# Performance work log

Hardware: AMD Instinct MI355X
Metric: run time of the kernel (lower is better)

The kernel has to match this reference:

```python
import jax, jax.numpy as jnp
import numpy as np

USER_NUM = 100000
ITEM_NUM = 100000
N = USER_NUM + ITEM_NUM
D = 64
N_EDGES = 3200000
N_LAYERS = 3
LAYER_CL = 1
EPS = 0.2


def setup_inputs() -> dict:
    key = jax.random.key(0)
    k1, k2, k3, k4, k5, k6 = jax.random.split(key, 6)
    user_emb = jax.random.normal(k1, (USER_NUM, D), dtype=jnp.float32)
    item_emb = jax.random.normal(k2, (ITEM_NUM, D), dtype=jnp.float32)
    adj_src = jax.random.randint(k3, (N_EDGES,), 0, N, dtype=jnp.int64)
    adj_dst = jax.random.randint(k4, (N_EDGES,), 0, N, dtype=jnp.int64)
    adj_vals = jax.random.uniform(k5, (N_EDGES,), dtype=jnp.float32)
    noise = jax.random.uniform(k6, (N_LAYERS, N, D), dtype=jnp.float32)
    return {"user_emb": user_emb, "item_emb": item_emb, "adj_src": adj_src,
            "adj_dst": adj_dst, "adj_vals": adj_vals, "noise": noise}


def reference(user_emb, item_emb, adj_src, adj_dst, adj_vals, noise):
    # ego_embeddings = cat([user_emb, item_emb])  -> [N, D]
    ego = jnp.concatenate([user_emb, item_emb], axis=0)
    acc = jnp.zeros_like(ego)
    cl = ego
    for k in range(N_LAYERS):
        # sparse.mm: out[dst] += val * ego[src]
        msg = ego[adj_src] * adj_vals[:, None]          # [E, D]
        ego = jax.ops.segment_sum(msg, adj_dst, num_segments=N)
        # perturbed noise injection: ego += sign(ego) * F.normalize(noise, dim=-1) * eps
        rn = noise[k]
        rn = rn / jnp.maximum(jnp.linalg.norm(rn, axis=-1, keepdims=True), 1e-12)
        ego = ego + jnp.sign(ego) * rn * EPS
        acc = acc + ego
        if k == LAYER_CL - 1:
            cl = ego
    final = acc / N_LAYERS  # mean over stacked layer outputs
    return (final[:USER_NUM], final[USER_NUM:], cl[:USER_NUM], cl[USER_NUM:])
```

## Files before the change

kernel.cpp:

```cpp
#include <hip/hip_runtime.h>

#define USER_NUM 100000
#define ITEM_NUM 100000
#define NN 200000
#define DIM 64
#define EPSV 0.2f

#define NB 196
#define BSH 10
#define NPB 1024
#define CH 4096
#define PER 16
#define SRC_MASK 0x3FFFF

__global__ __launch_bounds__(256) void bhist_k(const int* __restrict__ dst,
                                               int* __restrict__ bhist, int E) {
    __shared__ int h[NB];
    int t = threadIdx.x;
    for (int i = t; i < NB; i += 256) h[i] = 0;
    __syncthreads();
    long long base = (long long)blockIdx.x * CH;
    #pragma unroll
    for (int j = 0; j < PER; ++j) {
        long long e = base + t + j * 256;
        if (e < E) atomicAdd(&h[dst[e] >> BSH], 1);
    }
    __syncthreads();
    for (int i = t; i < NB; i += 256) if (h[i]) atomicAdd(&bhist[i], h[i]);
}

__global__ __launch_bounds__(256) void bscan_k(const int* __restrict__ bhist,
                                               int* __restrict__ bucket_base,
                                               int* __restrict__ bucket_off,
                                               int* __restrict__ row_ptr, int E) {
    __shared__ int tmp[256];
    int t = threadIdx.x;
    int s = (t < NB) ? bhist[t] : 0;
    tmp[t] = s;
    __syncthreads();
    for (int off = 1; off < 256; off <<= 1) {
        int x = (t >= off) ? tmp[t - off] : 0;
        __syncthreads();
        tmp[t] += x;
        __syncthreads();
    }
    int excl = tmp[t] - s;
    if (t < NB) { bucket_base[t] = excl; bucket_off[t] = excl; }
    if (t == 0) { bucket_base[NB] = E; row_ptr[NN] = E; }
}

__global__ __launch_bounds__(256) void apart_k(const int* __restrict__ src,
                                               const int* __restrict__ dst,
                                               const float* __restrict__ vals,
                                               int* __restrict__ bucket_off,
                                               int2* __restrict__ out, int E) {
    __shared__ int cnt[NB], start[NB], cursor[NB], gbase[NB];
    __shared__ int tmp[256];
    __shared__ int2 rec[CH];
    int t = threadIdx.x;
    long long base = (long long)blockIdx.x * CH;
    int nvalid = (int)min((long long)CH, (long long)E - base);

    int s_[PER]; int d_[PER]; float v_[PER];
    for (int i = t; i < NB; i += 256) cnt[i] = 0;
    __syncthreads();
    #pragma unroll
    for (int j = 0; j < PER; ++j) {
        int idx = t + j * 256;
        if (idx < nvalid) {
            long long e = base + idx;
            d_[j] = dst[e]; s_[j] = src[e]; v_[j] = vals[e];
            atomicAdd(&cnt[d_[j] >> BSH], 1);
        } else d_[j] = -1;
    }
    __syncthreads();
    int c = (t < NB) ? cnt[t] : 0;
    tmp[t] = c;
    __syncthreads();
    for (int off = 1; off < 256; off <<= 1) {
        int x = (t >= off) ? tmp[t - off] : 0;
        __syncthreads();
        tmp[t] += x;
        __syncthreads();
    }
    if (t < NB) {
        int excl = tmp[t] - c;
        start[t] = excl; cursor[t] = excl;
        gbase[t] = (c > 0) ? atomicAdd(&bucket_off[t], c) : 0;
    }
    __syncthreads();
    #pragma unroll
    for (int j = 0; j < PER; ++j) {
        if (d_[j] >= 0) {
            int b = d_[j] >> BSH;
            int slot = atomicAdd(&cursor[b], 1);
            rec[slot] = make_int2(s_[j] | ((d_[j] & (NPB - 1)) << 18),
                                  __float_as_int(v_[j]));
        }
    }
    __syncthreads();
    for (int slot = t; slot < nvalid; slot += 256) {
        int lo = 0, hi = NB - 1;
        while (lo < hi) {
            int mid = (lo + hi + 1) >> 1;
            if (start[mid] <= slot) lo = mid; else hi = mid - 1;
        }
        out[gbase[lo] + (slot - start[lo])] = rec[slot];
    }
}

__global__ __launch_bounds__(256) void bsort_k(const int* __restrict__ bucket_base,
                                               const int2* __restrict__ in,
                                               int2* __restrict__ out,
                                               int* __restrict__ row_ptr) {
    __shared__ int noff[NPB];
    __shared__ int tmp[256];
    int b = blockIdx.x, t = threadIdx.x;
    int rbeg = bucket_base[b], rend = bucket_base[b + 1];
    for (int i = t; i < NPB; i += 256) noff[i] = 0;
    __syncthreads();
    for (int i = rbeg + t; i < rend; i += 256)
        atomicAdd(&noff[(in[i].x >> 18) & (NPB - 1)], 1);
    __syncthreads();
    int l0 = noff[t * 4], l1 = noff[t * 4 + 1], l2 = noff[t * 4 + 2], l3 = noff[t * 4 + 3];
    int s = l0 + l1 + l2 + l3;
    tmp[t] = s;
    __syncthreads();
    for (int off = 1; off < 256; off <<= 1) {
        int x = (t >= off) ? tmp[t - off] : 0;
        __syncthreads();
        tmp[t] += x;
        __syncthreads();
    }
    int run = rbeg + tmp[t] - s;
    int e0 = run, e1 = run + l0, e2 = e1 + l1, e3 = e2 + l2;
    noff[t * 4] = e0; noff[t * 4 + 1] = e1; noff[t * 4 + 2] = e2; noff[t * 4 + 3] = e3;
    int node0 = b * NPB + t * 4;
    if (node0 < NN)     row_ptr[node0]     = e0;
    if (node0 + 1 < NN) row_ptr[node0 + 1] = e1;
    if (node0 + 2 < NN) row_ptr[node0 + 2] = e2;
    if (node0 + 3 < NN) row_ptr[node0 + 3] = e3;
    __syncthreads();
    for (int i = rbeg + t; i < rend; i += 256) {
        int2 r = in[i];
        int pos = atomicAdd(&noff[(r.x >> 18) & (NPB - 1)], 1);
        out[pos] = r;
    }
}

__global__ __launch_bounds__(256) void spmm_fused_k(const int* __restrict__ row_ptr,
                                                    const int2* __restrict__ ssv,
                                                    const float* __restrict__ ego_u,
                                                    const float* __restrict__ ego_i,
                                                    float* __restrict__ ego_out,
                                                    const float* __restrict__ nz_layer,
                                                    float* __restrict__ acc,
                                                    int is_first, int is_last) {
    int node = blockIdx.x * 4 + (threadIdx.x >> 6);
    int lane = threadIdx.x & 63;
    int beg = row_ptr[node];
    int end = row_ptr[node + 1];

    float a = 0.f;
    int base = beg;
    for (; base + 16 <= end; base += 16) {
        int2 sv = ssv[base + (lane & 15)];
        #pragma unroll
        for (int j = 0; j < 16; ++j) {
            int sj = __builtin_amdgcn_readlane(sv.x, j) & SRC_MASK;
            float vj = __int_as_float(__builtin_amdgcn_readlane(sv.y, j));
            const float* eb = (sj < USER_NUM) ? ego_u : ego_i;
            a += eb[(long long)sj * DIM + lane] * vj;
        }
    }
    int rem = end - base;
    if (rem > 0) {
        int i = base + (lane & 15);
        if (i >= end) i = end - 1;
        int2 sv = ssv[i];
        for (int j = 0; j < rem; ++j) {
            int sj = __builtin_amdgcn_readlane(sv.x, j) & SRC_MASK;
            float vj = __int_as_float(__builtin_amdgcn_readlane(sv.y, j));
            const float* eb = (sj < USER_NUM) ? ego_u : ego_i;
            a += eb[(long long)sj * DIM + lane] * vj;
        }
    }

    long long off = (long long)node * DIM + lane;
    float nz = nz_layer[off];
    float ss = nz * nz;
    #pragma unroll
    for (int o = 32; o > 0; o >>= 1) ss += __shfl_xor(ss, o, 64);
    float inv = 1.0f / fmaxf(sqrtf(ss), 1e-12f);
    float sgn = (a > 0.f) ? 1.f : ((a < 0.f) ? -1.f : 0.f);
    float val = a + sgn * nz * inv * EPSV;
    if (!is_last) ego_out[off] = val;
    float r = is_first ? val : (acc[off] + val);
    acc[off] = is_last ? r * (1.0f / 3.0f) : r;
}

extern "C" void kernel_launch(void* const* d_in, const int* in_sizes, int n_in,
                              void* d_out, int out_size, void* d_ws, size_t ws_size,
                              hipStream_t stream) {
    const float* user_emb = (const float*)d_in[0];
    const float* item_emb = (const float*)d_in[1];
    const int*   adj_src  = (const int*)d_in[2];
    const int*   adj_dst  = (const int*)d_in[3];
    const float* adj_vals = (const float*)d_in[4];
    const float* noise    = (const float*)d_in[5];
    const int E = in_sizes[2];

    const long long ND = (long long)NN * DIM;
    float* out_final = (float*)d_out;
    float* out_cl    = out_final + ND;

    char*  w       = (char*)d_ws;
    float* ego_a   = (float*)w;
    int2*  ssv_b   = (int2*)w;
    int2*  ssv     = (int2*)(w + ND * sizeof(float));
    int*   bhist   = (int*)(ssv + E);
    int*   bbase   = bhist + NB;
    int*   boff    = bbase + NB + 1;
    int*   row_ptr = boff + NB;

    const int nchunk = (E + CH - 1) / CH;

    hipMemsetAsync(bhist, 0, NB * sizeof(int), stream);
    bhist_k<<<nchunk, 256, 0, stream>>>(adj_dst, bhist, E);
    bscan_k<<<1, 256, 0, stream>>>(bhist, bbase, boff, row_ptr, E);
    apart_k<<<nchunk, 256, 0, stream>>>(adj_src, adj_dst, adj_vals, boff, ssv_b, E);
    bsort_k<<<NB, 256, 0, stream>>>(bbase, ssv_b, ssv, row_ptr);

    const int spmm_grid = NN / 4;
    const float* item_shift = item_emb - (long long)USER_NUM * DIM;
    spmm_fused_k<<<spmm_grid, 256, 0, stream>>>(row_ptr, ssv, user_emb, item_shift,
                                                out_cl, noise, out_final, 1, 0);
    spmm_fused_k<<<spmm_grid, 256, 0, stream>>>(row_ptr, ssv, out_cl, out_cl,
                                                ego_a, noise + ND, out_final, 0, 0);
    spmm_fused_k<<<spmm_grid, 256, 0, stream>>>(row_ptr, ssv, ego_a, ego_a,
                                                nullptr, noise + 2 * ND, out_final, 0, 1);
}
```

Measured before the change: 889.5 us.

## Split wave into four edge groups with float4 gathers and double accumulation

Restructures the SpMM inner loop so each 64-lane wave handles four edges at a time, with each 16-lane group gathering a full 64-float row through float4 loads. This replaces the per-edge readlane broadcast and scalar loads. Partial sums are combined with cross-group shuffles, and the epilogue uses float4 noise, ego and acc accesses written by one group. Accumulation is done in double precision, which raises FP64 FMA and register cost and changes rounding relative to the float reference.

```diff
diff --git a/kernel.cpp b/kernel.cpp
--- a/kernel.cpp
+++ b/kernel.cpp
@@ -158,45 +158,70 @@
                                                     int is_first, int is_last) {
     int node = blockIdx.x * 4 + (threadIdx.x >> 6);
     int lane = threadIdx.x & 63;
+    int g    = lane >> 4;
+    int d4   = lane & 15;
     int beg = row_ptr[node];
     int end = row_ptr[node + 1];
 
-    float a = 0.f;
+    double ax = 0.0, ay = 0.0, az = 0.0, aw = 0.0;
     int base = beg;
-    for (; base + 16 <= end; base += 16) {
-        int2 sv = ssv[base + (lane & 15)];
-        #pragma unroll
-        for (int j = 0; j < 16; ++j) {
-            int sj = __builtin_amdgcn_readlane(sv.x, j) & SRC_MASK;
-            float vj = __int_as_float(__builtin_amdgcn_readlane(sv.y, j));
-            const float* eb = (sj < USER_NUM) ? ego_u : ego_i;
-            a += eb[(long long)sj * DIM + lane] * vj;
-        }
+    #pragma unroll 2
+    for (; base + 4 <= end; base += 4) {
+        int2 sv = ssv[base + g];
+        int s = sv.x & SRC_MASK;
+        double v = (double)__int_as_float(sv.y);
+        const float* eb = (s < USER_NUM) ? ego_u : ego_i;
+        const float4 r = *reinterpret_cast<const float4*>(eb + ((size_t)s << 6) + (d4 << 2));
+        ax = fma((double)r.x, v, ax); ay = fma((double)r.y, v, ay);
+        az = fma((double)r.z, v, az); aw = fma((double)r.w, v, aw);
     }
     int rem = end - base;
-    if (rem > 0) {
-        int i = base + (lane & 15);
-        if (i >= end) i = end - 1;
-        int2 sv = ssv[i];
-        for (int j = 0; j < rem; ++j) {
-            int sj = __builtin_amdgcn_readlane(sv.x, j) & SRC_MASK;
-            float vj = __int_as_float(__builtin_amdgcn_readlane(sv.y, j));
-            const float* eb = (sj < USER_NUM) ? ego_u : ego_i;
-            a += eb[(long long)sj * DIM + lane] * vj;
-        }
-    }
-
-    long long off = (long long)node * DIM + lane;
-    float nz = nz_layer[off];
-    float ss = nz * nz;
-    #pragma unroll
-    for (int o = 32; o > 0; o >>= 1) ss += __shfl_xor(ss, o, 64);
-    float inv = 1.0f / fmaxf(sqrtf(ss), 1e-12f);
-    float sgn = (a > 0.f) ? 1.f : ((a < 0.f) ? -1.f : 0.f);
-    float val = a + sgn * nz * inv * EPSV;
-    if (!is_last) ego_out[off] = val;
-    float r = is_first ? val : (acc[off] + val);
-    acc[off] = is_last ? r * (1.0f / 3.0f) : r;
+    if (g < rem) {
+        int2 sv = ssv[base + g];
+        int s = sv.x & SRC_MASK;
+        double v = (double)__int_as_float(sv.y);
+        const float* eb = (s < USER_NUM) ? ego_u : ego_i;
+        const float4 r = *reinterpret_cast<const float4*>(eb + ((size_t)s << 6) + (d4 << 2));
+        ax = fma((double)r.x, v, ax); ay = fma((double)r.y, v, ay);
+        az = fma((double)r.z, v, az); aw = fma((double)r.w, v, aw);
+    }
+    ax += __shfl_xor(ax, 16, 64); ay += __shfl_xor(ay, 16, 64);
+    az += __shfl_xor(az, 16, 64); aw += __shfl_xor(aw, 16, 64);
+    ax += __shfl_xor(ax, 32, 64); ay += __shfl_xor(ay, 32, 64);
+    az += __shfl_xor(az, 32, 64); aw += __shfl_xor(aw, 32, 64);
+    float fx = (float)ax, fy = (float)ay, fz = (float)az, fw = (float)aw;
+
+    size_t off = (size_t)node * DIM + (d4 << 2);
+    const float4 nz = *reinterpret_cast<const float4*>(nz_layer + off);
+    float ss = nz.x * nz.x + nz.y * nz.y + nz.z * nz.z + nz.w * nz.w;
+    ss += __shfl_xor(ss, 1, 64);
+    ss += __shfl_xor(ss, 2, 64);
+    ss += __shfl_xor(ss, 4, 64);
+    ss += __shfl_xor(ss, 8, 64);
+    float e = EPSV / fmaxf(sqrtf(ss), 1e-12f);
+
+    float4 val;
+    val.x = fx + ((fx > 0.f) ? 1.f : ((fx < 0.f) ? -1.f : 0.f)) * nz.x * e;
+    val.y = fy + ((fy > 0.f) ? 1.f : ((fy < 0.f) ? -1.f : 0.f)) * nz.y * e;
+    val.z = fz + ((fz > 0.f) ? 1.f : ((fz < 0.f) ? -1.f : 0.f)) * nz.z * e;
+    val.w = fw + ((fw > 0.f) ? 1.f : ((fw < 0.f) ? -1.f : 0.f)) * nz.w * e;
+
+    if (g == 0) {
+        if (!is_last) *reinterpret_cast<float4*>(ego_out + off) = val;
+        float4 r4;
+        if (is_first) {
+            r4 = val;
+        } else {
+            const float4 p = *reinterpret_cast<const float4*>(acc + off);
+            r4.x = p.x + val.x; r4.y = p.y + val.y;
+            r4.z = p.z + val.z; r4.w = p.w + val.w;
+        }
+        if (is_last) {
+            r4.x *= (1.0f / 3.0f); r4.y *= (1.0f / 3.0f);
+            r4.z *= (1.0f / 3.0f); r4.w *= (1.0f / 3.0f);
+        }
+        *reinterpret_cast<float4*>(acc + off) = r4;
+    }
 }
 
 extern "C" void kernel_launch(void* const* d_in, const int* in_sizes, int n_in,
```

After: 793.6 us. -10.8%, faster.
